# Performance work log

Measured on AMD Instinct MI355X. Metric: run time of the kernel, lower is better.

Reference implementation:

```python
import jax, jax.numpy as jnp
import numpy as np

# Module hyperparameters (from init_kwargs)
MEAN = (0.485, 0.456, 0.406)
STD = (0.229, 0.224, 0.225)
P_ERASE = 0.5
SCALE = (0.02, 0.33)
RATIO = (0.3, 3.3)


def setup_inputs() -> dict:
    key = jax.random.key(0)
    x = jax.random.uniform(key, (64, 3, 384, 384), dtype=jnp.float32)
    mean = jnp.array(MEAN, dtype=jnp.float32).reshape(1, 3, 1, 1)
    std = jnp.array(STD, dtype=jnp.float32).reshape(1, 3, 1, 1)
    return {"x": x, "mean": mean, "std": std}


def reference(x, mean, std):
    """Normalize then apply batched random erasing (training mode).

    Faithful to the torch module, but the per-sample Python loop is replaced
    by a single vectorized mask computation over the whole batch.
    """
    B, C, H, W = x.shape
    xn = (x - mean) / std

    k = jax.random.key(42)
    kp, ka, kr, kt, kl, kn = jax.random.split(k, 6)

    # Per-sample: keep-or-erase coin flip, target area, aspect ratio.
    apply = jax.random.uniform(kp, (B,)) <= P_ERASE
    area = float(H * W)
    ta = jax.random.uniform(ka, (B,), minval=SCALE[0], maxval=SCALE[1]) * area
    ar = jax.random.uniform(kr, (B,), minval=RATIO[0], maxval=RATIO[1])
    h_e = jnp.round(jnp.sqrt(ta * ar)).astype(jnp.int32)
    w_e = jnp.round(jnp.sqrt(ta / ar)).astype(jnp.int32)
    valid = apply & (h_e < H) & (w_e < W)

    # Uniform integer top/left in [0, H-h_e] / [0, W-w_e] (matches randint high=H-h_e+1).
    top = jnp.floor(jax.random.uniform(kt, (B,)) * (H - h_e + 1).astype(jnp.float32)).astype(jnp.int32)
    left = jnp.floor(jax.random.uniform(kl, (B,)) * (W - w_e + 1).astype(jnp.float32)).astype(jnp.int32)

    rows = jnp.arange(H)[None, :]                       # (1, H)
    cols = jnp.arange(W)[None, :]                       # (1, W)
    rmask = (rows >= top[:, None]) & (rows < (top + h_e)[:, None])    # (B, H)
    cmask = (cols >= left[:, None]) & (cols < (left + w_e)[:, None])  # (B, W)
    mask = valid[:, None, None] & rmask[:, :, None] & cmask[:, None, :]  # (B, H, W)

    noise = jax.random.normal(kn, x.shape, dtype=x.dtype)
    return jnp.where(mask[:, None, :, :], noise, xn)
```

## Files before the change

kernel.cpp:

```cpp
#include <hip/hip_runtime.h>
#include <cstring>
#include <cstdint>
#include <cmath>

#define B_IMG 64
#define C_IMG 3
#define H_IMG 384
#define W_IMG 384
#define PLANE (H_IMG * W_IMG)
#define N_TOT (B_IMG * C_IMG * PLANE)
#define N4    (N_TOT / 4)
#define V4_PER_BLOCK 512
#define BLOCKS (N4 / V4_PER_BLOCK)

typedef float nfloat4 __attribute__((ext_vector_type(4)));

struct Rect { int t, b, l, r; };
struct Params { Rect rc[B_IMG]; };

__host__ __device__ inline uint32_t rotl32(uint32_t x, uint32_t r) {
  return (x << r) | (x >> (32u - r));
}

__host__ __device__ inline void tf2x32(uint32_t k0, uint32_t k1,
                                       uint32_t x0, uint32_t x1,
                                       uint32_t& o0, uint32_t& o1) {
  const uint32_t ks2 = k0 ^ k1 ^ 0x1BD11BDAu;
  x0 += k0; x1 += k1;
  x0 += x1; x1 = rotl32(x1, 13); x1 ^= x0;
  x0 += x1; x1 = rotl32(x1, 15); x1 ^= x0;
  x0 += x1; x1 = rotl32(x1, 26); x1 ^= x0;
  x0 += x1; x1 = rotl32(x1,  6); x1 ^= x0;
  x0 += k1; x1 += ks2 + 1u;
  x0 += x1; x1 = rotl32(x1, 17); x1 ^= x0;
  x0 += x1; x1 = rotl32(x1, 29); x1 ^= x0;
  x0 += x1; x1 = rotl32(x1, 16); x1 ^= x0;
  x0 += x1; x1 = rotl32(x1, 24); x1 ^= x0;
  x0 += ks2; x1 += k0 + 2u;
  x0 += x1; x1 = rotl32(x1, 13); x1 ^= x0;
  x0 += x1; x1 = rotl32(x1, 15); x1 ^= x0;
  x0 += x1; x1 = rotl32(x1, 26); x1 ^= x0;
  x0 += x1; x1 = rotl32(x1,  6); x1 ^= x0;
  x0 += k0; x1 += k1 + 3u;
  x0 += x1; x1 = rotl32(x1, 17); x1 ^= x0;
  x0 += x1; x1 = rotl32(x1, 29); x1 ^= x0;
  x0 += x1; x1 = rotl32(x1, 16); x1 ^= x0;
  x0 += x1; x1 = rotl32(x1, 24); x1 ^= x0;
  x0 += k1; x1 += ks2 + 4u;
  x0 += x1; x1 = rotl32(x1, 13); x1 ^= x0;
  x0 += x1; x1 = rotl32(x1, 15); x1 ^= x0;
  x0 += x1; x1 = rotl32(x1, 26); x1 ^= x0;
  x0 += x1; x1 = rotl32(x1,  6); x1 ^= x0;
  x0 += ks2; x1 += k0 + 5u;
  o0 = x0; o1 = x1;
}

__host__ __device__ inline float unit_from_bits(uint32_t bits) {
  uint32_t fb = (bits >> 9) | 0x3f800000u;
  float f;
#ifdef __HIP_DEVICE_COMPILE__
  f = __uint_as_float(fb);
#else
  memcpy(&f, &fb, 4);
#endif
  return f - 1.0f;
}

__host__ __device__ inline uint32_t rb_partitionable(uint32_t k0, uint32_t k1, uint32_t idx) {
  uint32_t o0, o1;
  tf2x32(k0, k1, 0u, idx, o0, o1);
  return o0 ^ o1;
}

__device__ inline float noise_val(uint32_t idx, uint32_t kn0, uint32_t kn1) {
  const float LO = -0x1.fffffep-1f;
  uint32_t bits = rb_partitionable(kn0, kn1, idx);
  float f = unit_from_bits(bits);
  float u = __fadd_rn(__fmul_rn(f, 2.0f), LO);
  u = fmaxf(LO, u);
  float t  = __fmul_rn(u, u);
  float wv = -log1pf(-t);
  float p;
  if (wv < 5.0f) {
    float ww = __fadd_rn(wv, -2.5f);
    p = 2.81022636e-08f;
    p = __fadd_rn(__fmul_rn(p, ww),  3.43273939e-07f);
    p = __fadd_rn(__fmul_rn(p, ww), -3.5233877e-06f);
    p = __fadd_rn(__fmul_rn(p, ww), -4.39150654e-06f);
    p = __fadd_rn(__fmul_rn(p, ww),  0.00021858087f);
    p = __fadd_rn(__fmul_rn(p, ww), -0.00125372503f);
    p = __fadd_rn(__fmul_rn(p, ww), -0.00417768164f);
    p = __fadd_rn(__fmul_rn(p, ww),  0.246640727f);
    p = __fadd_rn(__fmul_rn(p, ww),  1.50140941f);
  } else {
    float ww = __fadd_rn(__fsqrt_rn(wv), -3.0f);
    p = -0.000200214257f;
    p = __fadd_rn(__fmul_rn(p, ww),  0.000100950558f);
    p = __fadd_rn(__fmul_rn(p, ww),  0.00134934322f);
    p = __fadd_rn(__fmul_rn(p, ww), -0.00367342844f);
    p = __fadd_rn(__fmul_rn(p, ww),  0.00573950773f);
    p = __fadd_rn(__fmul_rn(p, ww), -0.0076224613f);
    p = __fadd_rn(__fmul_rn(p, ww),  0.00943887047f);
    p = __fadd_rn(__fmul_rn(p, ww),  1.00167406f);
    p = __fadd_rn(__fmul_rn(p, ww),  2.83297682f);
  }
  float r = __fmul_rn(p, u);
  return __fmul_rn(1.41421356237f, r);
}

static void compute_host_params(Params& P, uint32_t& kn0, uint32_t& kn1) {
#pragma clang fp contract(off)
  uint32_t keys[6][2];
  for (uint32_t i = 0; i < 6; i++)
    tf2x32(0u, 42u, 0u, i, keys[i][0], keys[i][1]);
  kn0 = keys[5][0]; kn1 = keys[5][1];

  for (int b = 0; b < B_IMG; b++) {
    float u[5];
    for (int k = 0; k < 5; k++)
      u[k] = unit_from_bits(rb_partitionable(keys[k][0], keys[k][1], (uint32_t)b));

    float up = u[0];
    float da = 0.33f - 0.02f;
    float ua = u[1] * da;  ua = ua + 0.02f;  ua = fmaxf(0.02f, ua);
    float ta = ua * 147456.0f;
    float dr = 3.3f - 0.3f;
    float ur = u[2] * dr;  ur = ur + 0.3f;   ur = fmaxf(0.3f, ur);

    int he = (int)rintf(sqrtf(ta * ur));
    int we = (int)rintf(sqrtf(ta / ur));
    bool valid = (up <= 0.5f) && (he < H_IMG) && (we < W_IMG);

    int top  = (int)floorf(u[3] * (float)(H_IMG - he + 1));
    int left = (int)floorf(u[4] * (float)(W_IMG - we + 1));

    if (valid) { P.rc[b].t = top;  P.rc[b].b = top + he; P.rc[b].l = left; P.rc[b].r = left + we; }
    else       { P.rc[b].t = 0;    P.rc[b].b = 0;        P.rc[b].l = 0;    P.rc[b].r = 0; }
  }
}

__global__ __launch_bounds__(256) void erase_norm_kernel(
    const float* __restrict__ x, const float* __restrict__ mean,
    const float* __restrict__ stdv, float* __restrict__ out,
    Params P, uint32_t kn0, uint32_t kn1) {
  const int t = threadIdx.x;
  const int bid = blockIdx.x;
  const int plane = bid / (PLANE / (V4_PER_BLOCK * 4));
  const int c = plane % C_IMG;
  const int b = plane / C_IMG;

  const nfloat4* __restrict__ x4 = reinterpret_cast<const nfloat4*>(x);
  nfloat4* __restrict__ o4 = reinterpret_cast<nfloat4*>(out);

  const int i0 = bid * V4_PER_BLOCK + t;
  const int i1 = i0 + 256;
  const nfloat4 v0 = __builtin_nontemporal_load(&x4[i0]);
  const nfloat4 v1 = __builtin_nontemporal_load(&x4[i1]);

  const float m  = mean[c];
  const float rs = 1.0f / stdv[c];
  const float nm = -m * rs;
  const Rect rc = P.rc[b];
  const int planeBase = plane * PLANE;

  const int blockStart = bid * (V4_PER_BLOCK * 4) - planeBase;
  const int h0 = blockStart / W_IMG;
  const int hN = (blockStart + V4_PER_BLOCK * 4 - 1) / W_IMG;

  nfloat4 o0, o1;
  o0.x = fmaf(v0.x, rs, nm);
  o0.y = fmaf(v0.y, rs, nm);
  o0.z = fmaf(v0.z, rs, nm);
  o0.w = fmaf(v0.w, rs, nm);
  o1.x = fmaf(v1.x, rs, nm);
  o1.y = fmaf(v1.y, rs, nm);
  o1.z = fmaf(v1.z, rs, nm);
  o1.w = fmaf(v1.w, rs, nm);

  if (rc.b > rc.t && hN >= rc.t && h0 < rc.b) {
    nfloat4 vv[2] = {o0, o1};
    int idx4[2] = {i0, i1};
#pragma unroll
    for (int j = 0; j < 2; j++) {
      nfloat4 o = vv[j];
      const int base = idx4[j] * 4;
      const int rel  = base - planeBase;
      const int h = rel / W_IMG;
      const int w = rel - h * W_IMG;
      if (h >= rc.t && h < rc.b && w < rc.r && (w + 3) >= rc.l) {
        if (w     >= rc.l && w     < rc.r) o.x = noise_val((uint32_t)(base + 0), kn0, kn1);
        if (w + 1 >= rc.l && w + 1 < rc.r) o.y = noise_val((uint32_t)(base + 1), kn0, kn1);
        if (w + 2 >= rc.l && w + 2 < rc.r) o.z = noise_val((uint32_t)(base + 2), kn0, kn1);
        if (w + 3 >= rc.l && w + 3 < rc.r) o.w = noise_val((uint32_t)(base + 3), kn0, kn1);
      }
      o4[idx4[j]] = o;
    }
  } else {
    o4[i0] = o0;
    o4[i1] = o1;
  }
}

extern "C" void kernel_launch(void* const* d_in, const int* in_sizes, int n_in,
                              void* d_out, int out_size, void* d_ws, size_t ws_size,
                              hipStream_t stream) {
  const float* x    = (const float*)d_in[0];
  const float* mean = (const float*)d_in[1];
  const float* stdv = (const float*)d_in[2];
  float* out = (float*)d_out;

  Params P;
  uint32_t kn0, kn1;
  compute_host_params(P, kn0, kn1);

  erase_norm_kernel<<<BLOCKS, 256, 0, stream>>>(x, mean, stdv, out, P, kn0, kn1);
}
```

Before: 199.6 us.

## Split erased-patch noise generation into dedicated blocks separate from normalization

```diff
diff --git a/kernel.cpp b/kernel.cpp
--- a/kernel.cpp
+++ b/kernel.cpp
@@ -12,6 +12,8 @@
 #define N4    (N_TOT / 4)
 #define V4_PER_BLOCK 512
 #define BLOCKS (N4 / V4_PER_BLOCK)
+#define PATCH_ROWGROUPS 8
+#define PATCH_BLOCKS (B_IMG * C_IMG * PATCH_ROWGROUPS)
 
 typedef float nfloat4 __attribute__((ext_vector_type(4)));
 
@@ -144,7 +146,26 @@
     const float* __restrict__ stdv, float* __restrict__ out,
     Params P, uint32_t kn0, uint32_t kn1) {
   const int t = threadIdx.x;
-  const int bid = blockIdx.x;
+
+  if (blockIdx.x < PATCH_BLOCKS) {
+    const int pb = blockIdx.x;
+    const int bc = pb % (B_IMG * C_IMG);
+    const int rg = pb / (B_IMG * C_IMG);
+    const int b = bc / C_IMG;
+    const Rect rc = P.rc[b];
+    if (rc.t == rc.b) return;
+    const int planeBase = bc * PLANE;
+    for (int h = rc.t + rg; h < rc.b; h += PATCH_ROWGROUPS) {
+      const int rowBase = planeBase + h * W_IMG;
+      for (int w = rc.l + t; w < rc.r; w += 256) {
+        const int idx = rowBase + w;
+        out[idx] = noise_val((uint32_t)idx, kn0, kn1);
+      }
+    }
+    return;
+  }
+
+  const int bid = blockIdx.x - PATCH_BLOCKS;
   const int plane = bid / (PLANE / (V4_PER_BLOCK * 4));
   const int c = plane % C_IMG;
   const int b = plane / C_IMG;
@@ -182,18 +203,19 @@
     int idx4[2] = {i0, i1};
 #pragma unroll
     for (int j = 0; j < 2; j++) {
-      nfloat4 o = vv[j];
+      const nfloat4 o = vv[j];
       const int base = idx4[j] * 4;
       const int rel  = base - planeBase;
       const int h = rel / W_IMG;
       const int w = rel - h * W_IMG;
       if (h >= rc.t && h < rc.b && w < rc.r && (w + 3) >= rc.l) {
-        if (w     >= rc.l && w     < rc.r) o.x = noise_val((uint32_t)(base + 0), kn0, kn1);
-        if (w + 1 >= rc.l && w + 1 < rc.r) o.y = noise_val((uint32_t)(base + 1), kn0, kn1);
-        if (w + 2 >= rc.l && w + 2 < rc.r) o.z = noise_val((uint32_t)(base + 2), kn0, kn1);
-        if (w + 3 >= rc.l && w + 3 < rc.r) o.w = noise_val((uint32_t)(base + 3), kn0, kn1);
+        if (!(w     >= rc.l && w     < rc.r)) out[base + 0] = o.x;
+        if (!(w + 1 >= rc.l && w + 1 < rc.r)) out[base + 1] = o.y;
+        if (!(w + 2 >= rc.l && w + 2 < rc.r)) out[base + 2] = o.z;
+        if (!(w + 3 >= rc.l && w + 3 < rc.r)) out[base + 3] = o.w;
+      } else {
+        o4[idx4[j]] = o;
       }
-      o4[idx4[j]] = o;
     }
   } else {
     o4[i0] = o0;
@@ -213,5 +235,5 @@
   uint32_t kn0, kn1;
   compute_host_params(P, kn0, kn1);
 
-  erase_norm_kernel<<<BLOCKS, 256, 0, stream>>>(x, mean, stdv, out, P, kn0, kn1);
-}
+  erase_norm_kernel<<<PATCH_BLOCKS + BLOCKS, 256, 0, stream>>>(x, mean, stdv, out, P, kn0, kn1);
+}
```

After: 217.9 us. 1.09x slower.
